# Kernel tuning notes

Hardware: AMD Instinct MI355X
Metric: run time of the kernel (lower is better)

## Reference

```python
import jax, jax.numpy as jnp
import numpy as np

SEQ, D, FF, E = 32768, 1024, 4096, 8
CAPACITY = int(1.25 * SEQ / E)  # 5120, matches int(capacity_factor*seq/n_experts)


def setup_inputs() -> dict:
    key = jax.random.key(0)
    ks = jax.random.split(key, 5)
    n = lambda k, shape, s: (jax.random.normal(k, shape, jnp.float32) * s)
    return {
        "x": n(ks[0], (SEQ, D), 1.0),
        "Wg": n(ks[1], (D, E), 0.02),          # router (switch) weight
        "bg": jnp.zeros((E,), jnp.float32),
        "W1": n(ks[2], (E, D, FF), 0.02),      # per-expert FFN in-proj
        "b1": jnp.zeros((E, FF), jnp.float32),
        "W2": n(ks[3], (E, FF, D), 0.02),      # per-expert FFN out-proj
        "b2": jnp.zeros((E, D), jnp.float32),
    }


def reference(x, Wg, bg, W1, b1, W2, b2):
    # --- Switch routing ---
    probs = jax.nn.softmax(x @ Wg + bg, axis=-1)            # [S,E]
    p_max = jnp.max(probs, axis=-1)                          # [S]
    routes = jnp.argmax(probs, axis=-1)                      # [S]

    # --- capacity-based dispatch (deterministic first-come-first-serve) ---
    onehot = jax.nn.one_hot(routes, E, dtype=jnp.int32)      # [S,E]
    pos = jnp.sum((jnp.cumsum(onehot, axis=0) - onehot) * onehot, axis=-1)  # slot within expert
    kept = pos < CAPACITY                                     # dropped tokens -> residual passthrough
    slot = jnp.where(kept, routes * CAPACITY + pos, E * CAPACITY)  # overflow bucket for dropped

    dispatch = jnp.zeros((E * CAPACITY + 1, D), x.dtype).at[slot].set(x)[:-1]
    einp = dispatch.reshape(E, CAPACITY, D)                   # [E,C,D] (zero-padded like F.pad)

    # --- per-expert BERT FFN (exact gelu) ---
    h = jax.nn.gelu(jnp.einsum('ecd,edf->ecf', einp, W1) + b1[:, None, :], approximate=False)
    eout = jnp.einsum('ecf,efd->ecd', h, W2) + b2[:, None, :]
    out_flat = eout.reshape(E * CAPACITY, D)

    # --- combine: scatter expert outputs back; dropped tokens keep x, factor 1.0 ---
    gathered = out_flat[jnp.minimum(slot, E * CAPACITY - 1)]
    final = jnp.where(kept[:, None], gathered, x)
    factor = jnp.where(kept, p_max, jnp.ones_like(p_max))
    # hidden_dropout_prob = 0.0 -> dropout is identity
    return final * factor[:, None]
```

## Files before the change

### kernel.cpp

```cpp
#include <hip/hip_runtime.h>
#include <stdint.h>

#define SEQ 32768
#define DIM 1024
#define FFD 4096
#define NE 8
#define CAP 5120

typedef __bf16 bf16x8 __attribute__((ext_vector_type(8)));
typedef float f32x4 __attribute__((ext_vector_type(4)));

__device__ __forceinline__ short f2bf(float f) {
  uint32_t u = __float_as_uint(f);
  uint32_t r = (u + 0x7fffu + ((u >> 16) & 1u)) >> 16;
  return (short)r;
}

__device__ __forceinline__ void async_copy16(const void* g, void* lds) {
  __builtin_amdgcn_global_load_lds((const __attribute__((address_space(1))) void*)g,
                                   (__attribute__((address_space(3))) void*)lds, 16, 0, 0);
}

__device__ __forceinline__ float gelu_tanh(float v) {
  float u = v * v;
  float z = v * fmaf(0.07135371f, u, 1.5957691f);
  float E = __expf(z);
  float R = __frcp_rn(1.0f + E);
  return fmaf(-v, R, v);
}

__global__ __launch_bounds__(256) void moe_router(const float* __restrict__ x,
                                                  const float* __restrict__ Wg,
                                                  const float* __restrict__ bg,
                                                  int* __restrict__ routes,
                                                  float* __restrict__ pmax) {
  int token = blockIdx.x * 4 + (threadIdx.x >> 6);
  int lane = threadIdx.x & 63;
  const float* xr = x + (size_t)token * DIM;
  double acc[NE];
#pragma unroll
  for (int e = 0; e < NE; e++) acc[e] = 0.0;
#pragma unroll
  for (int i = 0; i < DIM / 64; i++) {
    int d = i * 64 + lane;
    double xv = (double)xr[d];
    const float* wr = Wg + (size_t)d * NE;
    float4 w0 = *(const float4*)(wr);
    float4 w1 = *(const float4*)(wr + 4);
    acc[0] += xv * (double)w0.x; acc[1] += xv * (double)w0.y;
    acc[2] += xv * (double)w0.z; acc[3] += xv * (double)w0.w;
    acc[4] += xv * (double)w1.x; acc[5] += xv * (double)w1.y;
    acc[6] += xv * (double)w1.z; acc[7] += xv * (double)w1.w;
  }
#pragma unroll
  for (int e = 0; e < NE; e++) {
#pragma unroll
    for (int off = 32; off >= 1; off >>= 1) acc[e] += __shfl_xor(acc[e], off);
  }
  if (lane == 0) {
    double l[NE];
#pragma unroll
    for (int e = 0; e < NE; e++) l[e] = acc[e] + (double)bg[e];
    int am = 0;
#pragma unroll
    for (int e = 1; e < NE; e++) if (l[e] > l[am]) am = e;
    double s = 0.0;
#pragma unroll
    for (int e = 0; e < NE; e++) s += exp(l[e] - l[am]);
    routes[token] = am;
    pmax[token] = (float)(1.0 / s);
  }
}

__global__ __launch_bounds__(1024) void moe_scan(const int* __restrict__ routes,
                                                 int* __restrict__ slot_of_token,
                                                 int* __restrict__ token_of_slot,
                                                 int* __restrict__ counts) {
  __shared__ int wtot[16][NE];
  __shared__ int woff[16][NE];
  int t = threadIdx.x, lane = t & 63, w = t >> 6;
  int cnt[NE];
#pragma unroll
  for (int e = 0; e < NE; e++) cnt[e] = 0;
  int base = t * 32;
  for (int i = 0; i < 32; i++) {
    int r = routes[base + i];
#pragma unroll
    for (int e = 0; e < NE; e++) cnt[e] += (r == e) ? 1 : 0;
  }
  int incl[NE];
#pragma unroll
  for (int e = 0; e < NE; e++) {
    int v = cnt[e];
#pragma unroll
    for (int off = 1; off < 64; off <<= 1) {
      int o = __shfl_up(v, off);
      if (lane >= off) v += o;
    }
    incl[e] = v;
    if (lane == 63) wtot[w][e] = v;
  }
  __syncthreads();
  if (t < NE) {
    int run = 0;
    for (int ww = 0; ww < 16; ww++) {
      int tmp = wtot[ww][t];
      woff[ww][t] = run;
      run += tmp;
    }
    counts[t] = run;
  }
  __syncthreads();
  int pos[NE];
#pragma unroll
  for (int e = 0; e < NE; e++) pos[e] = woff[w][e] + incl[e] - cnt[e];
  for (int i = 0; i < 32; i++) {
    int tok = base + i;
    int r = routes[tok];
    int p = 0;
#pragma unroll
    for (int e = 0; e < NE; e++)
      if (r == e) { p = pos[e]; pos[e] = p + 1; }
    bool kept = p < CAP;
    int slot = kept ? r * CAP + p : NE * CAP;
    slot_of_token[tok] = slot;
    if (kept) token_of_slot[slot] = tok;
  }
}

__global__ __launch_bounds__(256) void moe_gather(const float* __restrict__ x,
                                                  const int* __restrict__ token_of_slot,
                                                  short* __restrict__ Xd) {
  int slot = blockIdx.x;
  int tok = token_of_slot[slot];
  int t = threadIdx.x;
  short* dst = Xd + (size_t)slot * DIM + t * 4;
  short4 v;
  if (tok < 0) {
    v.x = 0; v.y = 0; v.z = 0; v.w = 0;
  } else {
    float4 f = *(const float4*)(x + (size_t)tok * DIM + t * 4);
    v.x = f2bf(f.x); v.y = f2bf(f.y); v.z = f2bf(f.z); v.w = f2bf(f.w);
  }
  *(short4*)dst = v;
}

__global__ __launch_bounds__(256) void moe_convT(const float* __restrict__ W,
                                                 short* __restrict__ WT, int K, int N) {
  __shared__ float tile[32][33];
  int e = blockIdx.z;
  const float* We = W + (size_t)e * K * N;
  short* WTe = WT + (size_t)e * K * N;
  int n0 = blockIdx.x * 32, k0 = blockIdx.y * 32;
  int tx = threadIdx.x, ty = threadIdx.y;
#pragma unroll
  for (int i = 0; i < 4; i++)
    tile[ty + i * 8][tx] = We[(size_t)(k0 + ty + i * 8) * N + n0 + tx];
  __syncthreads();
#pragma unroll
  for (int i = 0; i < 4; i++)
    WTe[(size_t)(n0 + ty + i * 8) * K + k0 + tx] = f2bf(tile[tx][ty + i * 8]);
}


__device__ __forceinline__ void mainloop256(const short* __restrict__ Ag, int lda,
                                            const short* __restrict__ Bg, int ldb,
                                            int NT, short* smem, f32x4 acc[8][4],
                                            int wr, int wc, int l, int t) {
  const int cb = ((t & 7) << 4) ^ (((t >> 3) & 7) << 4);
  const int rs = t >> 3;
  const int rb = ((rs >> 5) << 6) + (rs & 31);
  const size_t la2 = (size_t)lda * 2, lb2 = (size_t)ldb * 2;
  const char* pa0q0 = (const char*)Ag + (size_t)(rs)       * la2 + cb;
  const char* pa0q1 = (const char*)Ag + (size_t)(128 + rs) * la2 + cb;
  const char* pa1q0 = (const char*)Ag + (size_t)(64 + rs)  * la2 + cb;
  const char* pa1q1 = (const char*)Ag + (size_t)(192 + rs) * la2 + cb;
  const char* pb0q0 = (const char*)Bg + (size_t)(rb)       * lb2 + cb;
  const char* pb0q1 = (const char*)Bg + (size_t)(128 + rb) * lb2 + cb;
  const char* pb1q0 = (const char*)Bg + (size_t)(32 + rb)  * lb2 + cb;
  const char* pb1q1 = (const char*)Bg + (size_t)(160 + rb) * lb2 + cb;
  short* dA = smem + t * 8;
  short* dB = smem + 32768 + t * 8;

  auto STG = [&](const char*& p0, const char*& p1, short* d) {
    async_copy16(p0, d);
    async_copy16(p1, d + 4096);
    p0 += 128; p1 += 128;
  };

  STG(pa0q0, pa0q1, dA);
  STG(pb0q0, pb0q1, dB);
  STG(pa1q0, pa1q1, dA + 8192);
  STG(pb1q0, pb1q1, dB + 8192);
  STG(pa0q0, pa0q1, dA + 16384);
  STG(pb0q0, pb0q1, dB + 16384);
  STG(pa1q0, pa1q1, dA + 16384 + 8192);
  asm volatile("s_waitcnt vmcnt(6)" ::: "memory");
  __builtin_amdgcn_s_barrier();

  const int l15 = l & 15;
  const int kh16 = (l >> 4) << 4;
  const int swz = (l15 & 7) << 4;
  const char* paK0 = (const char*)smem + (wr * 64 + l15) * 128 + (kh16 ^ swz);
  const char* paK1 = (const char*)smem + (wr * 64 + l15) * 128 + ((64 + kh16) ^ swz);
  const char* pbK0 = (const char*)smem + 65536 + (wc * 32 + l15) * 128 + (kh16 ^ swz);
  const char* pbK1 = (const char*)smem + 65536 + (wc * 32 + l15) * 128 + ((64 + kh16) ^ swz);

  for (int T = 0; T < NT; T++) {
    const int selByte = (T & 1) << 15;
    const int selSh = (T & 1) << 14;
    const int selShN = ((T + 1) & 1) << 14;
    const char* pa0 = paK0 + selByte;
    const char* pa1 = paK1 + selByte;
    const char* pb0 = pbK0 + selByte;
    const char* pb1 = pbK1 + selByte;
    bf16x8 a[4][2], b0[2][2], b1[2][2];
#pragma unroll
    for (int mf = 0; mf < 4; mf++) {
      a[mf][0] = *(const bf16x8*)(pa0 + mf * 2048);
      a[mf][1] = *(const bf16x8*)(pa1 + mf * 2048);
    }
#pragma unroll
    for (int nf = 0; nf < 2; nf++) {
      b0[nf][0] = *(const bf16x8*)(pb0 + nf * 2048);
      b0[nf][1] = *(const bf16x8*)(pb1 + nf * 2048);
    }
    if (T + 1 < NT) STG(pb1q0, pb1q1, dB + 8192 + selShN);
    __builtin_amdgcn_s_barrier();
    __builtin_amdgcn_s_setprio(1);
#pragma unroll
    for (int mf = 0; mf < 4; mf++)
#pragma unroll
      for (int nf = 0; nf < 2; nf++)
#pragma unroll
        for (int kk = 0; kk < 2; kk++)
          acc[mf][nf] = __builtin_amdgcn_mfma_f32_16x16x32_bf16(a[mf][kk], b0[nf][kk], acc[mf][nf], 0, 0, 0);
    __builtin_amdgcn_s_setprio(0);
    __builtin_amdgcn_s_barrier();
#pragma unroll
    for (int nf = 0; nf < 2; nf++) {
      b1[nf][0] = *(const bf16x8*)(pb0 + 16384 + nf * 2048);
      b1[nf][1] = *(const bf16x8*)(pb1 + 16384 + nf * 2048);
    }
    if (T + 2 < NT) STG(pa0q0, pa0q1, dA + selSh);
    __builtin_amdgcn_s_barrier();
    __builtin_amdgcn_s_setprio(1);
#pragma unroll
    for (int mf = 0; mf < 4; mf++)
#pragma unroll
      for (int nf = 0; nf < 2; nf++)
#pragma unroll
        for (int kk = 0; kk < 2; kk++)
          acc[mf][nf + 2] = __builtin_amdgcn_mfma_f32_16x16x32_bf16(a[mf][kk], b1[nf][kk], acc[mf][nf + 2], 0, 0, 0);
    __builtin_amdgcn_s_setprio(0);
    __builtin_amdgcn_s_barrier();
#pragma unroll
    for (int mf = 0; mf < 4; mf++) {
      a[mf][0] = *(const bf16x8*)(pa0 + 16384 + mf * 2048);
      a[mf][1] = *(const bf16x8*)(pa1 + 16384 + mf * 2048);
    }
    if (T + 2 < NT) STG(pb0q0, pb0q1, dB + selSh);
    __builtin_amdgcn_s_barrier();
    __builtin_amdgcn_s_setprio(1);
#pragma unroll
    for (int mf = 0; mf < 4; mf++)
#pragma unroll
      for (int nf = 0; nf < 2; nf++)
#pragma unroll
        for (int kk = 0; kk < 2; kk++)
          acc[mf + 4][nf + 2] = __builtin_amdgcn_mfma_f32_16x16x32_bf16(a[mf][kk], b1[nf][kk], acc[mf + 4][nf + 2], 0, 0, 0);
    __builtin_amdgcn_s_setprio(0);
    __builtin_amdgcn_s_barrier();
    if (T + 2 < NT) STG(pa1q0, pa1q1, dA + 8192 + selSh);
    __builtin_amdgcn_s_barrier();
    __builtin_amdgcn_s_setprio(1);
#pragma unroll
    for (int mf = 0; mf < 4; mf++)
#pragma unroll
      for (int nf = 0; nf < 2; nf++)
#pragma unroll
        for (int kk = 0; kk < 2; kk++)
          acc[mf + 4][nf] = __builtin_amdgcn_mfma_f32_16x16x32_bf16(a[mf][kk], b0[nf][kk], acc[mf + 4][nf], 0, 0, 0);
    __builtin_amdgcn_s_setprio(0);
    if (T + 2 < NT) asm volatile("s_waitcnt vmcnt(6)" ::: "memory");
    else            asm volatile("s_waitcnt vmcnt(0)" ::: "memory");
    __builtin_amdgcn_s_barrier();
  }
  asm volatile("s_waitcnt vmcnt(0) lgkmcnt(0)" ::: "memory");
  __builtin_amdgcn_s_barrier();
}

#define PITCH1 272
__global__ __launch_bounds__(512, 2) void moe_gemm1(const short* __restrict__ Xd,
                                                    const short* __restrict__ W1bT,
                                                    const float* __restrict__ b1,
                                                    short* __restrict__ h,
                                                    const int* __restrict__ counts,
                                                    int m_base, int rows, int mch) {
  extern __shared__ short smem[];
  int bid = blockIdx.x;
  int xcd = bid & 7;
  int idx = bid >> 3;
  int nn = idx & 15;
  int mlin = (idx >> 4) * 8 + xcd;
  int e = mlin / mch;
  int mm = mlin - e * mch;
  int cnt = counts[e]; if (cnt > CAP) cnt = CAP;
  int m0 = m_base + mm * 256;
  if (m0 >= cnt) return;
  int n0 = nn * 256;
  int t = threadIdx.x, l = t & 63, wid = t >> 6;
  int wr = wid >> 2, wc = wid & 3;
  const short* Ag = Xd + ((size_t)e * CAP + m0) * DIM;
  const short* Bg = W1bT + ((size_t)e * FFD + n0) * DIM;
  f32x4 acc[8][4];
#pragma unroll
  for (int mf = 0; mf < 8; mf++)
#pragma unroll
    for (int nf = 0; nf < 4; nf++) acc[mf][nf] = (f32x4){0.f, 0.f, 0.f, 0.f};
  mainloop256(Ag, DIM, Bg, DIM, DIM / 64, smem, acc, wr, wc, l, t);

  int l15 = l & 15, q4 = (l >> 4) * 4;
  float bias[4];
#pragma unroll
  for (int nf = 0; nf < 4; nf++)
    bias[nf] = b1[(size_t)e * FFD + n0 + wc * 64 + nf * 16 + l15];
#pragma unroll
  for (int half = 0; half < 2; half++) {
    if (wr == half) {
#pragma unroll
      for (int mf = 0; mf < 8; mf++)
#pragma unroll
        for (int nf = 0; nf < 4; nf++)
#pragma unroll
          for (int j = 0; j < 4; j++) {
            int lr = mf * 16 + q4 + j;
            int lc = wc * 64 + nf * 16 + l15;
            float v = acc[mf][nf][j] + bias[nf];
            smem[lr * PITCH1 + lc] = f2bf(gelu_tanh(v));
          }
    }
    asm volatile("s_waitcnt lgkmcnt(0)" ::: "memory");
    __builtin_amdgcn_s_barrier();
    int r = t >> 2, c0 = (t & 3) * 64;
    short* hrow = h + ((size_t)e * rows + (m0 - m_base) + half * 128 + r) * FFD + n0 + c0;
    const short* srow = smem + r * PITCH1 + c0;
#pragma unroll
    for (int i = 0; i < 8; i++)
      *(int4*)(hrow + i * 8) = *(const int4*)(srow + i * 8);
    asm volatile("s_waitcnt lgkmcnt(0)" ::: "memory");
    __builtin_amdgcn_s_barrier();
  }
}

__global__ __launch_bounds__(512, 2) void moe_gemm2(const short* __restrict__ h,
                                                    const short* __restrict__ W2bT,
                                                    const float* __restrict__ b2,
                                                    const int* __restrict__ token_of_slot,
                                                    const float* __restrict__ pmax,
                                                    float* __restrict__ out,
                                                    const int* __restrict__ counts,
                                                    int m_base, int rows, int mch) {
  extern __shared__ short smem[];
  int bid = blockIdx.x;
  int xcd = bid & 7;
  int idx = bid >> 3;
  int nn = idx & 3;
  int mlin = (idx >> 2) * 8 + xcd;
  int e = mlin / mch;
  int mm = mlin - e * mch;
  int cnt = counts[e]; if (cnt > CAP) cnt = CAP;
  int m0 = m_base + mm * 256;
  if (m0 >= cnt) return;
  int n0 = nn * 256;
  int t = threadIdx.x, l = t & 63, wid = t >> 6;
  int wr = wid >> 2, wc = wid & 3;
  const short* Ag = h + ((size_t)e * rows + (m0 - m_base)) * FFD;
  const short* Bg = W2bT + ((size_t)e * DIM + n0) * FFD;
  f32x4 acc[8][4];
#pragma unroll
  for (int mf = 0; mf < 8; mf++)
#pragma unroll
    for (int nf = 0; nf < 4; nf++) acc[mf][nf] = (f32x4){0.f, 0.f, 0.f, 0.f};
  mainloop256(Ag, FFD, Bg, FFD, FFD / 64, smem, acc, wr, wc, l, t);

  float* ftile = (float*)smem;
  int l15 = l & 15, q4 = (l >> 4) * 4;
  float bias[4];
#pragma unroll
  for (int nf = 0; nf < 4; nf++)
    bias[nf] = b2[(size_t)e * DIM + n0 + wc * 64 + nf * 16 + l15];
#pragma unroll
  for (int half = 0; half < 2; half++) {
    if (wr == half) {
#pragma unroll
      for (int mf = 0; mf < 8; mf++)
#pragma unroll
        for (int nf = 0; nf < 4; nf++)
#pragma unroll
          for (int j = 0; j < 4; j++) {
            int lr = mf * 16 + q4 + j;
            int lc = wc * 64 + nf * 16 + l15;
            ftile[lr * 256 + lc] = acc[mf][nf][j] + bias[nf];
          }
    }
    asm volatile("s_waitcnt lgkmcnt(0)" ::: "memory");
    __builtin_amdgcn_s_barrier();
    int r = t >> 2, c0 = (t & 3) * 64;
    int slotrow = m0 + half * 128 + r;
    int tok = token_of_slot[e * CAP + slotrow];
    if (tok >= 0) {
      float f = pmax[tok];
      float* orow = out + (size_t)tok * DIM + n0 + c0;
      const float* srow = ftile + r * 256 + c0;
#pragma unroll
      for (int i = 0; i < 16; i++) {
        float4 v = *(const float4*)(srow + i * 4);
        v.x *= f; v.y *= f; v.z *= f; v.w *= f;
        *(float4*)(orow + i * 4) = v;
      }
    }
    asm volatile("s_waitcnt lgkmcnt(0)" ::: "memory");
    __builtin_amdgcn_s_barrier();
  }
}

__global__ __launch_bounds__(256) void moe_fixup(const float* __restrict__ x,
                                                 const int* __restrict__ slot_of_token,
                                                 float* __restrict__ out) {
  int tok8 = blockIdx.x * 8 + (threadIdx.x >> 5);
  int lane32 = threadIdx.x & 31;
  if (slot_of_token[tok8] != NE * CAP) return;
#pragma unroll
  for (int i = 0; i < 8; i++) {
    int c = (i * 32 + lane32) * 4;
    float4 v = *(const float4*)(x + (size_t)tok8 * DIM + c);
    *(float4*)(out + (size_t)tok8 * DIM + c) = v;
  }
}

extern "C" void kernel_launch(void* const* d_in, const int* in_sizes, int n_in,
                              void* d_out, int out_size, void* d_ws, size_t ws_size,
                              hipStream_t stream) {
  (void)in_sizes; (void)n_in; (void)out_size;
  const float* x  = (const float*)d_in[0];
  const float* Wg = (const float*)d_in[1];
  const float* bg = (const float*)d_in[2];
  const float* W1 = (const float*)d_in[3];
  const float* b1 = (const float*)d_in[4];
  const float* W2 = (const float*)d_in[5];
  const float* b2 = (const float*)d_in[6];
  float* out = (float*)d_out;

  static bool attr_set = false;
  if (!attr_set) {
    hipFuncSetAttribute((const void*)moe_gemm1, hipFuncAttributeMaxDynamicSharedMemorySize, 131072);
    hipFuncSetAttribute((const void*)moe_gemm2, hipFuncAttributeMaxDynamicSharedMemorySize, 131072);
    attr_set = true;
  }

  char* p = (char*)d_ws;
  auto carve = [&](size_t bytes) -> char* {
    char* r = p;
    p += (bytes + 255) & ~(size_t)255;
    return r;
  };
  short* W1bT = (short*)carve((size_t)NE * DIM * FFD * 2);
  short* W2bT = (short*)carve((size_t)NE * DIM * FFD * 2);
  short* Xd   = (short*)carve((size_t)NE * CAP * DIM * 2);
  int* routes = (int*)carve((size_t)SEQ * 4);
  float* pmax = (float*)carve((size_t)SEQ * 4);
  int* slot_of_token = (int*)carve((size_t)SEQ * 4);
  int* token_of_slot = (int*)carve((size_t)(NE * CAP) * 4);
  int* counts = (int*)carve(256);
  size_t fixed = (size_t)(p - (char*)d_ws);

  size_t avail = (ws_size > fixed + 4096) ? (ws_size - fixed - 4096) : 0;
  size_t per_row = (size_t)NE * FFD * 2;
  int rows = (int)(avail / per_row);
  rows &= ~255;
  if (rows > CAP) rows = CAP;
  if (rows < 256) rows = 256;
  short* h = (short*)p;

  hipMemsetAsync(token_of_slot, 0xFF, (size_t)(NE * CAP) * 4, stream);
  moe_router<<<SEQ / 4, 256, 0, stream>>>(x, Wg, bg, routes, pmax);
  moe_scan<<<1, 1024, 0, stream>>>(routes, slot_of_token, token_of_slot, counts);
  moe_gather<<<NE * CAP, 256, 0, stream>>>(x, token_of_slot, Xd);
  moe_convT<<<dim3(FFD / 32, DIM / 32, NE), dim3(32, 8), 0, stream>>>(W1, W1bT, DIM, FFD);
  moe_convT<<<dim3(DIM / 32, FFD / 32, NE), dim3(32, 8), 0, stream>>>(W2, W2bT, FFD, DIM);

  for (int r0 = 0; r0 < CAP; r0 += rows) {
    int cr = (CAP - r0 < rows) ? (CAP - r0) : rows;
    int mch = cr / 256;
    moe_gemm1<<<16 * NE * mch, 512, 131072, stream>>>(Xd, W1bT, b1, h, counts, r0, rows, mch);
    moe_gemm2<<<4 * NE * mch, 512, 131072, stream>>>(h, W2bT, b2, token_of_slot, pmax, out,
                                                     counts, r0, rows, mch);
  }
  moe_fixup<<<SEQ / 8, 256, 0, stream>>>(x, slot_of_token, out);
}
```

Before: 1.071 ms.

## Load B operand directly from global into registers in FFN1 GEMM mainloop

Adds a mainloop variant for the first expert GEMM that stages only the A tile (dispatched tokens) through LDS via async copies. Each wave reads its B (W1 transposed) fragments straight from global memory into registers every k-step. This halves LDS traffic and footprint for the tile. In exchange, each wave issues uncoalesced-ish global loads for B with no cross-wave reuse, and those loads sit on the critical path with no prefetch, so latency may stall the MFMAs.

```diff
diff --git a/kernel.cpp b/kernel.cpp
--- a/kernel.cpp
+++ b/kernel.cpp
@@ -162,6 +162,118 @@
     WTe[(size_t)(n0 + ty + i * 8) * K + k0 + tx] = f2bf(tile[tx][ty + i * 8]);
 }
 
+__device__ __forceinline__ void mainloop256_regB(const short* __restrict__ Ag, int lda,
+                                                 const short* __restrict__ Bg, int ldb,
+                                                 int NT, short* smem, f32x4 acc[8][4],
+                                                 int wr, int wc, int l, int t) {
+  const int cb = ((t & 7) << 4) ^ (((t >> 3) & 7) << 4);
+  const int rs = t >> 3;
+  const size_t la2 = (size_t)lda * 2;
+  const char* pa0q0 = (const char*)Ag + (size_t)(rs)       * la2 + cb;
+  const char* pa0q1 = (const char*)Ag + (size_t)(128 + rs) * la2 + cb;
+  const char* pa1q0 = (const char*)Ag + (size_t)(64 + rs)  * la2 + cb;
+  const char* pa1q1 = (const char*)Ag + (size_t)(192 + rs) * la2 + cb;
+  short* dA = smem + t * 8;
+
+  auto STG = [&](const char*& p0, const char*& p1, short* d) {
+    async_copy16(p0, d);
+    async_copy16(p1, d + 4096);
+    p0 += 128; p1 += 128;
+  };
+
+  STG(pa0q0, pa0q1, dA);
+  STG(pa1q0, pa1q1, dA + 8192);
+  STG(pa0q0, pa0q1, dA + 16384);
+  STG(pa1q0, pa1q1, dA + 16384 + 8192);
+  asm volatile("s_waitcnt vmcnt(4)" ::: "memory");
+  __builtin_amdgcn_s_barrier();
+
+  const int l15 = l & 15;
+  const int kh16 = (l >> 4) << 4;
+  const int swz = (l15 & 7) << 4;
+  const char* paK0 = (const char*)smem + (wr * 64 + l15) * 128 + (kh16 ^ swz);
+  const char* paK1 = (const char*)smem + (wr * 64 + l15) * 128 + ((64 + kh16) ^ swz);
+  const size_t lb2 = (size_t)ldb * 2;
+  const char* pbG = (const char*)Bg + (size_t)(wc * 64 + l15) * lb2 + kh16;
+  const size_t nfOff = (size_t)16 * lb2;
+  const size_t b1Off = (size_t)32 * lb2;
+
+  for (int T = 0; T < NT; T++) {
+    const int selByte = (T & 1) << 15;
+    const int selSh = (T & 1) << 14;
+    const char* pa0 = paK0 + selByte;
+    const char* pa1 = paK1 + selByte;
+    bf16x8 a[4][2], b0[2][2], b1[2][2];
+#pragma unroll
+    for (int nf = 0; nf < 2; nf++)
+#pragma unroll
+      for (int kk = 0; kk < 2; kk++) {
+        b0[nf][kk] = *(const bf16x8*)(pbG + nf * nfOff + kk * 64);
+        b1[nf][kk] = *(const bf16x8*)(pbG + b1Off + nf * nfOff + kk * 64);
+      }
+#pragma unroll
+    for (int mf = 0; mf < 4; mf++) {
+      a[mf][0] = *(const bf16x8*)(pa0 + mf * 2048);
+      a[mf][1] = *(const bf16x8*)(pa1 + mf * 2048);
+    }
+    __builtin_amdgcn_s_barrier();
+    __builtin_amdgcn_s_setprio(1);
+#pragma unroll
+    for (int mf = 0; mf < 4; mf++)
+#pragma unroll
+      for (int nf = 0; nf < 2; nf++)
+#pragma unroll
+        for (int kk = 0; kk < 2; kk++)
+          acc[mf][nf] = __builtin_amdgcn_mfma_f32_16x16x32_bf16(a[mf][kk], b0[nf][kk], acc[mf][nf], 0, 0, 0);
+    __builtin_amdgcn_s_setprio(0);
+    __builtin_amdgcn_s_barrier();
+    if (T + 2 < NT) STG(pa0q0, pa0q1, dA + selSh);
+    __builtin_amdgcn_s_barrier();
+    __builtin_amdgcn_s_setprio(1);
+#pragma unroll
+    for (int mf = 0; mf < 4; mf++)
+#pragma unroll
+      for (int nf = 0; nf < 2; nf++)
+#pragma unroll
+        for (int kk = 0; kk < 2; kk++)
+          acc[mf][nf + 2] = __builtin_amdgcn_mfma_f32_16x16x32_bf16(a[mf][kk], b1[nf][kk], acc[mf][nf + 2], 0, 0, 0);
+    __builtin_amdgcn_s_setprio(0);
+    __builtin_amdgcn_s_barrier();
+#pragma unroll
+    for (int mf = 0; mf < 4; mf++) {
+      a[mf][0] = *(const bf16x8*)(pa0 + 16384 + mf * 2048);
+      a[mf][1] = *(const bf16x8*)(pa1 + 16384 + mf * 2048);
+    }
+    __builtin_amdgcn_s_barrier();
+    __builtin_amdgcn_s_setprio(1);
+#pragma unroll
+    for (int mf = 0; mf < 4; mf++)
+#pragma unroll
+      for (int nf = 0; nf < 2; nf++)
+#pragma unroll
+        for (int kk = 0; kk < 2; kk++)
+          acc[mf + 4][nf + 2] = __builtin_amdgcn_mfma_f32_16x16x32_bf16(a[mf][kk], b1[nf][kk], acc[mf + 4][nf + 2], 0, 0, 0);
+    __builtin_amdgcn_s_setprio(0);
+    __builtin_amdgcn_s_barrier();
+    if (T + 2 < NT) STG(pa1q0, pa1q1, dA + 8192 + selSh);
+    __builtin_amdgcn_s_barrier();
+    __builtin_amdgcn_s_setprio(1);
+#pragma unroll
+    for (int mf = 0; mf < 4; mf++)
+#pragma unroll
+      for (int nf = 0; nf < 2; nf++)
+#pragma unroll
+        for (int kk = 0; kk < 2; kk++)
+          acc[mf + 4][nf] = __builtin_amdgcn_mfma_f32_16x16x32_bf16(a[mf][kk], b0[nf][kk], acc[mf + 4][nf], 0, 0, 0);
+    __builtin_amdgcn_s_setprio(0);
+    if (T + 2 < NT) asm volatile("s_waitcnt vmcnt(4)" ::: "memory");
+    else            asm volatile("s_waitcnt vmcnt(0)" ::: "memory");
+    __builtin_amdgcn_s_barrier();
+    pbG += 128;
+  }
+  asm volatile("s_waitcnt vmcnt(0) lgkmcnt(0)" ::: "memory");
+  __builtin_amdgcn_s_barrier();
+}
 
 __device__ __forceinline__ void mainloop256(const short* __restrict__ Ag, int lda,
                                             const short* __restrict__ Bg, int ldb,
@@ -318,7 +430,7 @@
   for (int mf = 0; mf < 8; mf++)
 #pragma unroll
     for (int nf = 0; nf < 4; nf++) acc[mf][nf] = (f32x4){0.f, 0.f, 0.f, 0.f};
-  mainloop256(Ag, DIM, Bg, DIM, DIM / 64, smem, acc, wr, wc, l, t);
+  mainloop256_regB(Ag, DIM, Bg, DIM, DIM / 64, smem, acc, wr, wc, l, t);
 
   int l15 = l & 15, q4 = (l >> 4) * 4;
   float bias[4];
```

After: 1.263 ms. +17.9%, slower.
